# Kernel optimization log

Measured on AMD Instinct MI355X. Metric: run time of the kernel, lower is better.

Reference implementation:

```python
import math
import jax, jax.numpy as jnp
import numpy as np

B, M, N = 32, 64, 5000   # batch, multi_width (POMO rollouts), n_nodes
L, H, D, E = 100, 8, 16, 128  # local_size, head_num, qkv_dim, emb_dim


def setup_inputs() -> dict:
    key = jax.random.key(0)
    ks = jax.random.split(key, 10)
    return {
        "dist": jax.random.uniform(ks[0], (B, M, N), jnp.float32),
        "theta": jax.random.uniform(ks[1], (B, M, N), jnp.float32, minval=-math.pi, maxval=math.pi),
        "ninf_mask": jnp.zeros((B, M, N), jnp.float32),
        "W_init": jax.random.normal(ks[2], (E, 2), jnp.float32) * 0.1,
        "b_init": jax.random.normal(ks[3], (E,), jnp.float32) * 0.1,
        "cur_token": jax.random.uniform(ks[4], (E,), jnp.float32, minval=-1.0, maxval=1.0),
        "Wq": jax.random.normal(ks[5], (H * D, E), jnp.float32) * 0.05,
        "Wk": jax.random.normal(ks[6], (H * D, E), jnp.float32) * 0.05,
        "Wv": jax.random.normal(ks[7], (H * D, E), jnp.float32) * 0.05,
        "Wc": jax.random.normal(ks[8], (E, H * D), jnp.float32) * 0.05,
        "bc": jax.random.normal(ks[9], (E,), jnp.float32) * 0.05,
    }


def _positional_signal():
    # transformer sinusoidal encoding over the L gathered neighbors (E even -> no pad)
    num_ts = E // 2
    log_inc = math.log(10000.0) / max(num_ts - 1, 1)
    inv_ts = jnp.exp(jnp.arange(num_ts, dtype=jnp.float32) * -log_inc)
    pos = jnp.arange(L, dtype=jnp.float32)
    scaled = pos[:, None] * inv_ts[None, :]            # [L, E/2]
    return jnp.concatenate([jnp.sin(scaled), jnp.cos(scaled)], axis=1)  # [L, E]


def reference(dist, theta, ninf_mask, W_init, b_init, cur_token, Wq, Wk, Wv, Wc, bc):
    # mask out infeasible nodes (dist - (-inf) = +inf pushes them out of top-k)
    d = dist - ninf_mask                               # [B, M, N]
    neg_vals, idx = jax.lax.top_k(-d, L)               # smallest-L distances
    sorted_dist = -neg_vals                            # [B, M, L] ascending
    sorted_mask = jnp.take_along_axis(ninf_mask, idx, axis=-1)
    norm = sorted_dist.max(axis=-1, keepdims=True) + 1e-6
    sorted_dist = sorted_dist / norm
    sorted_theta = jnp.take_along_axis(theta, idx, axis=-1)
    sdt = jnp.stack([sorted_dist, sorted_theta], axis=-1)   # [B, M, L, 2]

    init_k = sdt @ W_init.T + b_init + _positional_signal()  # [B, M, L, E]

    # current-token query is a single shared learned vector -> q is [H, D]
    q = (Wq @ cur_token).reshape(H, D)
    kh = (init_k @ Wk.T).reshape(B, M, L, H, D)
    vh = (init_k @ Wv.T).reshape(B, M, L, H, D)

    score = jnp.einsum('hd,bmlhd->bhml', q, kh) / jnp.sqrt(jnp.float32(D))
    score = score + sorted_mask[:, None, :, :]              # rank3 ninf mask
    w = jax.nn.softmax(score, axis=-1)                      # [B, H, M, L]
    att = jnp.einsum('bhml,bmlhd->bmhd', w, vh).reshape(B, M, H * D)
    mh = att @ Wc.T + bc                                    # [B, M, E]

    score2 = jnp.einsum('bme,bmle->bml', mh, init_k) / jnp.sqrt(jnp.float32(E))

    # scatter local scores back into full [B, M, N]
    bi = jnp.arange(B)[:, None, None]
    mi = jnp.arange(M)[None, :, None]
    out = jnp.zeros((B, M, N), jnp.float32).at[bi, mi, idx].set(score2)
    return out
```

## Files before the change

### kernel.cpp

```cpp
#include <hip/hip_runtime.h>
#include <math.h>

#define B_ 32
#define M_ 64
#define N_ 5000
#define L_ 100
#define H_ 8
#define D_ 16
#define E_ 128
#define NBIN 1024
#define NI4 1250
#define RPB 8

#define OFF_POSQ  0
#define OFF_C0    800
#define OFF_C1    808
#define OFF_C2    816
#define OFF_PV0   824
#define OFF_PV1   952
#define OFF_PVB   1080
#define OFF_WC0   1208
#define OFF_WC1   1336
#define OFF_WCB   1464
#define OFF_SB    1592
#define OFF_PCB   1596
#define OFF_PV    1696
#define OFF_PCT   14496

#define WSYNC() do { asm volatile("s_waitcnt lgkmcnt(0)" ::: "memory"); __builtin_amdgcn_sched_barrier(0); } while (0)
#define VSYNC() do { asm volatile("s_waitcnt vmcnt(0)" ::: "memory"); __builtin_amdgcn_sched_barrier(0); } while (0)

__device__ __forceinline__ int vbin(float v) {
  if (!(v >= 0.f)) return 0;
  if (v >= 1.0f) return NBIN - 1;
  return (int)(v * (float)NBIN);
}
__device__ __forceinline__ unsigned int umap(float v) {
  unsigned int b = __float_as_uint(v);
  return (b & 0x80000000u) ? ~b : (b | 0x80000000u);
}
#define HMAP(b)  ((((b) & 15) << 6) + ((b) >> 4))
#define HMAP4(b) ((((b) & 3) << 6) + ((b) >> 2))

__global__ __launch_bounds__(128) void precomp(
    const float* __restrict__ Wq, const float* __restrict__ Wk,
    const float* __restrict__ cur, const float* __restrict__ Wi,
    const float* __restrict__ bi, const float* __restrict__ Wv,
    const float* __restrict__ Wc, const float* __restrict__ bc,
    float* __restrict__ ws)
{
  const int tid = threadIdx.x;
  const int blk = blockIdx.x;
  __shared__ float pr[E_];
  __shared__ float red[8];
  const int lane = tid & 63, wvv = tid >> 6;

  if (blk == 0) {
    float qsv = 0.f;
    for (int e = 0; e < E_; ++e) qsv = fmaf(Wq[tid * E_ + e], cur[e], qsv);
    float wk0=0,wk1=0,wkb=0,pv0=0,pv1=0,pvb=0,wc0=0,wc1=0,wcb=0;
    for (int e = 0; e < E_; ++e) {
      float wi0 = Wi[2*e], wi1 = Wi[2*e+1], bie = bi[e];
      float wk = Wk[tid*E_+e], wvx = Wv[tid*E_+e], wcc = Wc[e*(H_*D_)+tid];
      wk0=fmaf(wk,wi0,wk0);  wk1=fmaf(wk,wi1,wk1);  wkb=fmaf(wk,bie,wkb);
      pv0=fmaf(wvx,wi0,pv0); pv1=fmaf(wvx,wi1,pv1); pvb=fmaf(wvx,bie,pvb);
      wc0=fmaf(wcc,wi0,wc0); wc1=fmaf(wcc,wi1,wc1); wcb=fmaf(wcc,bie,wcb);
    }
    ws[OFF_PV0+tid]=pv0; ws[OFF_PV1+tid]=pv1; ws[OFF_PVB+tid]=pvb;
    ws[OFF_WC0+tid]=wc0; ws[OFF_WC1+tid]=wc1; ws[OFF_WCB+tid]=wcb;
    float c0 = qsv*wk0, c1 = qsv*wk1, c2 = qsv*wkb;
    for (int off = 1; off < 16; off <<= 1) {
      c0 += __shfl_xor(c0, off, 16); c1 += __shfl_xor(c1, off, 16); c2 += __shfl_xor(c2, off, 16);
    }
    if ((tid & 15) == 0) {
      int h = tid >> 4;
      ws[OFF_C0+h] = c0*0.25f; ws[OFF_C1+h] = c1*0.25f; ws[OFF_C2+h] = c2*0.25f;
    }
    float p0 = Wi[2*tid]*bc[tid], p1 = Wi[2*tid+1]*bc[tid], p2 = bi[tid]*bc[tid];
    for (int off = 32; off > 0; off >>= 1) {
      p0 += __shfl_xor(p0, off, 64); p1 += __shfl_xor(p1, off, 64); p2 += __shfl_xor(p2, off, 64);
    }
    if (lane == 0) { red[wvv*3+0]=p0; red[wvv*3+1]=p1; red[wvv*3+2]=p2; }
    __syncthreads();
    if (tid == 0) {
      ws[OFF_SB+0]=red[0]+red[3]; ws[OFF_SB+1]=red[1]+red[4]; ws[OFF_SB+2]=red[2]+red[5];
    }
  } else {
    const int l = blk - 1;
    const float log_inc = 0.14619588050755848f;
    {
      int j = tid & 63;
      float scaled = (float)l * expf(-(float)j * log_inc);
      pr[tid] = (tid < 64) ? sinf(scaled) : cosf(scaled);
    }
    __syncthreads();
    float qsv=0.f, pwk=0.f, accv=0.f, accc=0.f;
    for (int e = 0; e < E_; ++e) qsv = fmaf(Wq[tid*E_+e], cur[e], qsv);
    for (int e = 0; e < E_; ++e) {
      float p = pr[e];
      pwk  = fmaf(Wk[tid*E_+e], p, pwk);
      accv = fmaf(Wv[tid*E_+e], p, accv);
      accc = fmaf(Wc[e*(H_*D_)+tid], p, accc);
    }
    ws[OFF_PV  + l*(H_*D_) + tid] = accv;
    ws[OFF_PCT + tid*L_ + l] = accc;
    float pq = qsv * pwk;
    for (int off = 1; off < 16; off <<= 1) pq += __shfl_xor(pq, off, 16);
    if ((tid & 15) == 0) ws[OFF_POSQ + (tid>>4)*L_ + l] = pq * 0.25f;
    float pb = pr[tid] * bc[tid];
    for (int off = 32; off > 0; off >>= 1) pb += __shfl_xor(pb, off, 64);
    if (lane == 0) red[wvv] = pb;
    __syncthreads();
    if (tid == 0) ws[OFF_PCB + l] = red[0] + red[1];
  }
}

__global__ __launch_bounds__(512) void local_att_kernel(
    const float* __restrict__ dist, const float* __restrict__ theta,
    const float* __restrict__ ninf, const float* __restrict__ ws,
    float* __restrict__ out)
{
  __shared__ alignas(16) unsigned int arena[RPB][1024];
  __shared__ unsigned int cnt8[RPB];

  const int tid  = threadIdx.x;
  const int lane = tid & 63;
  const int wv   = tid >> 6;
  const size_t base = (size_t)(blockIdx.x * RPB + wv) * N_;
  unsigned int* hist = arena[wv];
  unsigned long long* sel = (unsigned long long*)&arena[wv][256];
  float* sdv = (float*)&arena[wv][520];
  unsigned int* idxs = &arena[wv][648];
  float* stv = (float*)&arena[wv][776];
  float* smv = (float*)&arena[wv][876];
  float* att = (float*)&arena[wv][0];

  const float4* d4 = (const float4*)(dist + base);
  const float4* n4 = (const float4*)(ninf + base);

#pragma unroll
  for (int k = 0; k < 16; ++k) hist[lane + 64 * k] = 0u;
  WSYNC();

  {
    float4 dreg[20], nreg[20];
#pragma unroll
    for (int t = 0; t < 20; ++t) {
      int i4 = lane + 64 * t;
      if (i4 < NI4) { dreg[t] = d4[i4]; nreg[t] = n4[i4]; }
    }
#pragma unroll
    for (int t = 0; t < 20; ++t) {
      int i4 = lane + 64 * t;
      if (i4 < NI4) {
#pragma unroll
        for (int c = 0; c < 4; ++c) {
          float v = (&dreg[t].x)[c] - (&nreg[t].x)[c];
          atomicAdd(&hist[HMAP(vbin(v))], 1u);
        }
      }
    }
  }
  WSYNC();

  unsigned int bstar, cumB, binc;
  {
    unsigned int s = 0;
#pragma unroll
    for (int k = 0; k < 16; ++k) s += hist[k * 64 + lane];
    unsigned int v = s;
#pragma unroll
    for (int off = 1; off < 64; off <<= 1) {
      unsigned int x = __shfl_up(v, off, 64);
      if (lane >= off) v += x;
    }
    unsigned int cumBefore = v - s;
    bool cross = (cumBefore < (unsigned)L_) && (v >= (unsigned)L_);
    unsigned long long mk = __ballot(cross);
    int src = __ffsll(mk) - 1;
    unsigned int bstarL = 0, cumL = 0, bincL = 0;
    if (cross) {
      unsigned int c = cumBefore; int kk = 0;
      for (; kk < 16; ++kk) {
        unsigned int h = hist[kk * 64 + lane];
        if (c + h >= (unsigned)L_) { bincL = h; break; }
        c += h;
      }
      bstarL = (unsigned)(lane * 16 + kk); cumL = c;
    }
    bstar = (unsigned)__shfl((int)bstarL, src, 64);
    cumB  = (unsigned)__shfl((int)cumL,  src, 64);
    binc  = (unsigned)__shfl((int)bincL, src, 64);
  }
  const bool fb = (cumB + binc > 128u);

  if (!fb) {
    sel[lane] = ~0ull; sel[lane + 64] = ~0ull;
    if (lane == 0) cnt8[wv] = 0u;
    WSYNC();
    float4 dreg[20], nreg[20];
#pragma unroll
    for (int t = 0; t < 20; ++t) {
      int i4 = lane + 64 * t;
      if (i4 < NI4) { dreg[t] = d4[i4]; nreg[t] = n4[i4]; }
    }
#pragma unroll
    for (int t = 0; t < 20; ++t) {
      int i4 = lane + 64 * t;
      if (i4 < NI4) {
#pragma unroll
        for (int c = 0; c < 4; ++c) {
          float v = (&dreg[t].x)[c] - (&nreg[t].x)[c];
          if (vbin(v) <= (int)bstar) {
            unsigned long long key = ((unsigned long long)umap(v) << 16) | (unsigned)(i4 * 4 + c);
            unsigned int p = atomicAdd(&cnt8[wv], 1u);
            if (p < 128u) sel[p] = key;
          }
        }
      }
    }
  } else {
    unsigned long long prefix = 0ull;
    unsigned int Krem = L_;
    for (int pass = 0; pass < 6; ++pass) {
      const int shift = 40 - 8 * pass;
#pragma unroll
      for (int k = 0; k < 4; ++k) hist[lane + 64 * k] = 0u;
      WSYNC();
      for (int t = 0; t < 20; ++t) {
        int i4 = lane + 64 * t;
        if (i4 < NI4) {
          float4 dv = d4[i4], nv = n4[i4];
#pragma unroll
          for (int c = 0; c < 4; ++c) {
            float v = (&dv.x)[c] - (&nv.x)[c];
            unsigned long long key = ((unsigned long long)umap(v) << 16) | (unsigned)(i4 * 4 + c);
            if ((key >> (shift + 8)) == prefix)
              atomicAdd(&hist[HMAP4((int)((key >> shift) & 0xFFu))], 1u);
          }
        }
      }
      WSYNC();
      unsigned int s4 = 0;
#pragma unroll
      for (int k = 0; k < 4; ++k) s4 += hist[k * 64 + lane];
      unsigned int v2 = s4;
#pragma unroll
      for (int off = 1; off < 64; off <<= 1) {
        unsigned int x = __shfl_up(v2, off, 64);
        if (lane >= off) v2 += x;
      }
      unsigned int cb = v2 - s4;
      bool cr = (cb < Krem) && (v2 >= Krem);
      unsigned long long mk2 = __ballot(cr);
      int sl = __ffsll(mk2) - 1;
      unsigned int chL = 0, cmL = 0;
      if (cr) {
        unsigned int c = cb; int kk = 0;
        for (; kk < 4; ++kk) {
          unsigned int h = hist[kk * 64 + lane];
          if (c + h >= Krem) break;
          c += h;
        }
        chL = (unsigned)(lane * 4 + kk); cmL = c;
      }
      unsigned int chosen = (unsigned)__shfl((int)chL, sl, 64);
      unsigned int cum2   = (unsigned)__shfl((int)cmL, sl, 64);
      prefix = (prefix << 8) | chosen;
      Krem -= cum2;
      WSYNC();
    }
    const unsigned long long kpiv = prefix;
    sel[lane] = ~0ull; sel[lane + 64] = ~0ull;
    if (lane == 0) cnt8[wv] = 0u;
    WSYNC();
    for (int t = 0; t < 20; ++t) {
      int i4 = lane + 64 * t;
      if (i4 < NI4) {
        float4 dv = d4[i4], nv = n4[i4];
#pragma unroll
        for (int c = 0; c < 4; ++c) {
          float v = (&dv.x)[c] - (&nv.x)[c];
          unsigned long long key = ((unsigned long long)umap(v) << 16) | (unsigned)(i4 * 4 + c);
          if (key <= kpiv) {
            unsigned int p = atomicAdd(&cnt8[wv], 1u);
            if (p < 128u) sel[p] = key;
          }
        }
      }
    }
  }
  WSYNC();

  {
    unsigned long long ka = sel[lane], kb = sel[lane + 64];
    int ra = 0, rb = 0;
#pragma unroll 8
    for (int j2 = 0; j2 < 128; ++j2) {
      unsigned long long kj = sel[j2];
      ra += (kj < ka) ? 1 : 0;
      rb += (kj < kb) ? 1 : 0;
    }
    if (ka != ~0ull) {
      unsigned int u = (unsigned int)(ka >> 16);
      unsigned int bits = (u & 0x80000000u) ? (u ^ 0x80000000u) : ~u;
      sdv[ra] = __uint_as_float(bits);
      idxs[ra] = (unsigned int)(ka & 0xFFFFull);
    }
    if (kb != ~0ull) {
      unsigned int u = (unsigned int)(kb >> 16);
      unsigned int bits = (u & 0x80000000u) ? (u ^ 0x80000000u) : ~u;
      sdv[rb] = __uint_as_float(bits);
      idxs[rb] = (unsigned int)(kb & 0xFFFFull);
    }
  }
  WSYNC();

  const float invn = 1.0f / (sdv[L_ - 1] + 1e-6f);
  {
    const int l1 = lane + 64;
    const int l1g = (l1 < L_) ? l1 : 0;
    unsigned int i0 = idxs[lane], i1 = idxs[l1g];
    float sd0 = sdv[lane], sd1 = sdv[l1g];
    float th0 = theta[base + i0];
    float nm0 = ninf[base + i0];
    float th1 = 0.f, nm1 = 0.f;
    if (l1 < L_) { th1 = theta[base + i1]; nm1 = ninf[base + i1]; }
    stv[lane] = th0; smv[lane] = nm0; sdv[lane] = sd0 * invn;
    if (l1 < L_) { stv[l1] = th1; smv[l1] = nm1; sdv[l1] = sd1 * invn; }
  }
  WSYNC();

  const int hh = lane >> 3, jj = lane & 7;
  float w13[13];
  float a0, a1;
  {
    const float c0 = ws[OFF_C0 + hh], c1 = ws[OFF_C1 + hh], c2 = ws[OFF_C2 + hh];
    float mx = -INFINITY;
#pragma unroll
    for (int k = 0; k < 13; ++k) {
      int l = jj + 8 * k;
      float scv = -INFINITY;
      if (l < L_)
        scv = fmaf(sdv[l], c0, fmaf(stv[l], c1, c2 + ws[OFF_POSQ + hh * L_ + l] + smv[l]));
      w13[k] = scv;
      mx = fmaxf(mx, scv);
    }
#pragma unroll
    for (int off = 1; off <= 4; off <<= 1) mx = fmaxf(mx, __shfl_xor(mx, off, 64));
    float sum = 0.f;
#pragma unroll
    for (int k = 0; k < 13; ++k) { float e = expf(w13[k] - mx); w13[k] = e; sum += e; }
#pragma unroll
    for (int off = 1; off <= 4; off <<= 1) sum += __shfl_xor(sum, off, 64);
    const float inv = 1.0f / sum;
    a0 = 0.f; a1 = 0.f;
#pragma unroll
    for (int k = 0; k < 13; ++k) {
      int l = jj + 8 * k; int lc = (l < L_) ? l : 0;
      float wgt = w13[k] * inv; w13[k] = wgt;
      a0 = fmaf(wgt, sdv[lc], a0);
      a1 = fmaf(wgt, stv[lc], a1);
    }
#pragma unroll
    for (int off = 1; off <= 4; off <<= 1) { a0 += __shfl_xor(a0, off, 64); a1 += __shfl_xor(a1, off, 64); }
  }

  {
    float part[16];
#pragma unroll
    for (int t = 0; t < 16; ++t) part[t] = 0.f;
#pragma unroll
    for (int k = 0; k < 13; ++k) {
      int l = jj + 8 * k;
      if (l < L_) {
        const float* pv = ws + OFF_PV + l * (H_ * D_) + hh * 16;
        float wgt = w13[k];
#pragma unroll
        for (int t = 0; t < 16; ++t) part[t] = fmaf(wgt, pv[t], part[t]);
      }
    }
#pragma unroll
    for (int off = 1; off <= 4; off <<= 1) {
#pragma unroll
      for (int t = 0; t < 16; ++t) part[t] += __shfl_xor(part[t], off, 64);
    }
#pragma unroll
    for (int t = 0; t < 16; ++t) {
      int hd = hh * 16 + t;
      att[hd] = fmaf(a0, ws[OFF_PV0 + hd], fmaf(a1, ws[OFF_PV1 + hd], ws[OFF_PVB + hd])) + part[t];
    }
  }
  WSYNC();

  float m0, m1, mb;
  {
    float x0 = att[lane], x1 = att[lane + 64];
    m0 = fmaf(x0, ws[OFF_WC0 + lane], x1 * ws[OFF_WC0 + lane + 64]);
    m1 = fmaf(x0, ws[OFF_WC1 + lane], x1 * ws[OFF_WC1 + lane + 64]);
    mb = fmaf(x0, ws[OFF_WCB + lane], x1 * ws[OFF_WCB + lane + 64]);
#pragma unroll
    for (int off = 1; off < 64; off <<= 1) {
      m0 += __shfl_xor(m0, off, 64);
      m1 += __shfl_xor(m1, off, 64);
      mb += __shfl_xor(mb, off, 64);
    }
    m0 += ws[OFF_SB + 0]; m1 += ws[OFF_SB + 1]; mb += ws[OFF_SB + 2];
  }

  const int l1 = lane + 64;
  const int l1c = (l1 < L_) ? l1 : 0;
  float s2a = 0.f, s2b = 0.f;
#pragma unroll 8
  for (int hd = 0; hd < H_ * D_; ++hd) {
    float a = att[hd];
    s2a = fmaf(a, ws[OFF_PCT + hd * L_ + lane], s2a);
    s2b = fmaf(a, ws[OFF_PCT + hd * L_ + l1c], s2b);
  }
  const float SC = 0.08838834764831845f;
  float out_a = (fmaf(sdv[lane], m0, fmaf(stv[lane], m1, mb)) + ws[OFF_PCB + lane] + s2a) * SC;
  float out_b = (fmaf(sdv[l1c], m0, fmaf(stv[l1c], m1, mb)) + ws[OFF_PCB + l1c] + s2b) * SC;
  unsigned int ia = idxs[lane];
  unsigned int ib = idxs[l1c];

  {
    float4* o4 = (float4*)(out + base);
    const float4 z = make_float4(0.f, 0.f, 0.f, 0.f);
#pragma unroll
    for (int t = 0; t < 20; ++t) {
      int i4 = lane + 64 * t;
      if (i4 < NI4) o4[i4] = z;
    }
  }
  VSYNC();
  out[base + ia] = out_a;
  if (l1 < L_) out[base + ib] = out_b;
}

extern "C" void kernel_launch(void* const* d_in, const int* in_sizes, int n_in,
                              void* d_out, int out_size, void* d_ws, size_t ws_size,
                              hipStream_t stream) {
  const float* dist = (const float*)d_in[0];
  const float* theta = (const float*)d_in[1];
  const float* ninf = (const float*)d_in[2];
  const float* Wi   = (const float*)d_in[3];
  const float* bi   = (const float*)d_in[4];
  const float* cur  = (const float*)d_in[5];
  const float* Wq   = (const float*)d_in[6];
  const float* Wk   = (const float*)d_in[7];
  const float* Wv   = (const float*)d_in[8];
  const float* Wc   = (const float*)d_in[9];
  const float* bcv  = (const float*)d_in[10];
  float* out = (float*)d_out;
  float* ws  = (float*)d_ws;

  precomp<<<dim3(L_ + 1), dim3(128), 0, stream>>>(Wq, Wk, cur, Wi, bi, Wv, Wc, bcv, ws);
  local_att_kernel<<<dim3((B_ * M_) / RPB), dim3(512), 0, stream>>>(dist, theta, ninf, ws, out);
}
```

Measured before the change: 79.76 us.

## Process one row per 128-thread block with register-cached keys and single-pass output

The main kernel now gives each row a 128-thread block instead of one wave per row in a 512-thread block. Each thread keeps the mapped distance keys in registers, so the selection and fallback radix passes no longer reload dist and ninf from global memory. Output is written in one pass: a shared bitmap and hash table merge the scattered scores with the zero fill, replacing a zero store followed by scattered stores. The cost is block-wide barriers and shared atomics in place of wave-local sync, plus more registers per thread.

Measured after the change: 72.08 us. 1.11x faster.

```diff
diff --git a/kernel.cpp b/kernel.cpp
--- a/kernel.cpp
+++ b/kernel.cpp
@@ -10,7 +10,7 @@
 #define E_ 128
 #define NBIN 1024
 #define NI4 1250
-#define RPB 8
+#define NT 128
 
 #define OFF_POSQ  0
 #define OFF_C0    800
@@ -27,9 +27,6 @@
 #define OFF_PV    1696
 #define OFF_PCT   14496
 
-#define WSYNC() do { asm volatile("s_waitcnt lgkmcnt(0)" ::: "memory"); __builtin_amdgcn_sched_barrier(0); } while (0)
-#define VSYNC() do { asm volatile("s_waitcnt vmcnt(0)" ::: "memory"); __builtin_amdgcn_sched_barrier(0); } while (0)
-
 __device__ __forceinline__ int vbin(float v) {
   if (!(v >= 0.f)) return 0;
   if (v >= 1.0f) return NBIN - 1;
@@ -39,8 +36,12 @@
   unsigned int b = __float_as_uint(v);
   return (b & 0x80000000u) ? ~b : (b | 0x80000000u);
 }
-#define HMAP(b)  ((((b) & 15) << 6) + ((b) >> 4))
-#define HMAP4(b) ((((b) & 3) << 6) + ((b) >> 2))
+__device__ __forceinline__ float unmap(unsigned int u) {
+  unsigned int b = (u & 0x80000000u) ? (u ^ 0x80000000u) : ~u;
+  return __uint_as_float(b);
+}
+#define HMAP8(b) ((((b) & 7) << 7) | ((b) >> 3))
+#define HMAP2(b) ((((b) & 1) << 7) | ((b) >> 1))
 
 __global__ __launch_bounds__(128) void precomp(
     const float* __restrict__ Wq, const float* __restrict__ Wk,
@@ -115,106 +116,89 @@
   }
 }
 
-__global__ __launch_bounds__(512) void local_att_kernel(
+__global__ __launch_bounds__(NT, 4) void local_att_kernel(
     const float* __restrict__ dist, const float* __restrict__ theta,
     const float* __restrict__ ninf, const float* __restrict__ ws,
     float* __restrict__ out)
 {
-  __shared__ alignas(16) unsigned int arena[RPB][1024];
-  __shared__ unsigned int cnt8[RPB];
-
-  const int tid  = threadIdx.x;
-  const int lane = tid & 63;
-  const int wv   = tid >> 6;
-  const size_t base = (size_t)(blockIdx.x * RPB + wv) * N_;
-  unsigned int* hist = arena[wv];
-  unsigned long long* sel = (unsigned long long*)&arena[wv][256];
-  float* sdv = (float*)&arena[wv][520];
-  unsigned int* idxs = &arena[wv][648];
-  float* stv = (float*)&arena[wv][776];
-  float* smv = (float*)&arena[wv][876];
-  float* att = (float*)&arena[wv][0];
-
+  __shared__ unsigned int hist[NBIN];
+  __shared__ unsigned long long sel[128];
+  __shared__ float sdv[128];
+  __shared__ unsigned int idxs[128];
+  __shared__ float stv[L_], smv[L_];
+  __shared__ float att[H_ * D_];
+  __shared__ unsigned int bitmap[160];
+  __shared__ unsigned int hidx[256];
+  __shared__ float hval[256];
+  __shared__ unsigned int wsum[2];
+  __shared__ unsigned int s_bstar, s_cumB, s_binc, s_cnt, s_chosen, s_cumb2;
+
+  const int tid = threadIdx.x;
+  const int lane = tid & 63, wv = tid >> 6;
+  const size_t base = (size_t)blockIdx.x * N_;
   const float4* d4 = (const float4*)(dist + base);
   const float4* n4 = (const float4*)(ninf + base);
 
-#pragma unroll
-  for (int k = 0; k < 16; ++k) hist[lane + 64 * k] = 0u;
-  WSYNC();
-
-  {
-    float4 dreg[20], nreg[20];
-#pragma unroll
-    for (int t = 0; t < 20; ++t) {
-      int i4 = lane + 64 * t;
-      if (i4 < NI4) { dreg[t] = d4[i4]; nreg[t] = n4[i4]; }
-    }
-#pragma unroll
-    for (int t = 0; t < 20; ++t) {
-      int i4 = lane + 64 * t;
-      if (i4 < NI4) {
-#pragma unroll
-        for (int c = 0; c < 4; ++c) {
-          float v = (&dreg[t].x)[c] - (&nreg[t].x)[c];
-          atomicAdd(&hist[HMAP(vbin(v))], 1u);
-        }
-      }
-    }
-  }
-  WSYNC();
-
-  unsigned int bstar, cumB, binc;
+  for (int j = tid; j < NBIN; j += NT) hist[j] = 0u;
+  sel[tid] = ~0ull;
+  if (tid == 0) s_cnt = 0u;
+  __syncthreads();
+
+  unsigned int u[40];
+#pragma unroll
+  for (int t = 0; t < 10; ++t) {
+    int i4 = tid + NT * t;
+    if (i4 < NI4) {
+      float4 dv = d4[i4], nv = n4[i4];
+#pragma unroll
+      for (int c = 0; c < 4; ++c) {
+        float v = (&dv.x)[c] - (&nv.x)[c];
+        u[4 * t + c] = umap(v);
+        atomicAdd(&hist[HMAP8(vbin(v))], 1u);
+      }
+    }
+  }
+  __syncthreads();
+
   {
     unsigned int s = 0;
 #pragma unroll
-    for (int k = 0; k < 16; ++k) s += hist[k * 64 + lane];
+    for (int k = 0; k < 8; ++k) s += hist[(k << 7) | tid];
     unsigned int v = s;
 #pragma unroll
     for (int off = 1; off < 64; off <<= 1) {
       unsigned int x = __shfl_up(v, off, 64);
       if (lane >= off) v += x;
     }
+    if (lane == 63) wsum[wv] = v;
+    __syncthreads();
+    if (wv == 1) v += wsum[0];
     unsigned int cumBefore = v - s;
-    bool cross = (cumBefore < (unsigned)L_) && (v >= (unsigned)L_);
-    unsigned long long mk = __ballot(cross);
-    int src = __ffsll(mk) - 1;
-    unsigned int bstarL = 0, cumL = 0, bincL = 0;
-    if (cross) {
-      unsigned int c = cumBefore; int kk = 0;
-      for (; kk < 16; ++kk) {
-        unsigned int h = hist[kk * 64 + lane];
-        if (c + h >= (unsigned)L_) { bincL = h; break; }
+    if (cumBefore < (unsigned)L_ && v >= (unsigned)L_) {
+      unsigned int c = cumBefore;
+#pragma unroll
+      for (int k = 0; k < 8; ++k) {
+        unsigned int h = hist[(k << 7) | tid];
+        if (c + h >= (unsigned)L_) { s_bstar = tid * 8 + k; s_cumB = c; s_binc = h; break; }
         c += h;
       }
-      bstarL = (unsigned)(lane * 16 + kk); cumL = c;
-    }
-    bstar = (unsigned)__shfl((int)bstarL, src, 64);
-    cumB  = (unsigned)__shfl((int)cumL,  src, 64);
-    binc  = (unsigned)__shfl((int)bincL, src, 64);
-  }
-  const bool fb = (cumB + binc > 128u);
+    }
+    __syncthreads();
+  }
+  const int bstar = (int)s_bstar;
+  const bool fb = (s_cumB + s_binc > 128u);
 
   if (!fb) {
-    sel[lane] = ~0ull; sel[lane + 64] = ~0ull;
-    if (lane == 0) cnt8[wv] = 0u;
-    WSYNC();
-    float4 dreg[20], nreg[20];
-#pragma unroll
-    for (int t = 0; t < 20; ++t) {
-      int i4 = lane + 64 * t;
-      if (i4 < NI4) { dreg[t] = d4[i4]; nreg[t] = n4[i4]; }
-    }
-#pragma unroll
-    for (int t = 0; t < 20; ++t) {
-      int i4 = lane + 64 * t;
+#pragma unroll
+    for (int t = 0; t < 10; ++t) {
+      int i4 = tid + NT * t;
       if (i4 < NI4) {
 #pragma unroll
         for (int c = 0; c < 4; ++c) {
-          float v = (&dreg[t].x)[c] - (&nreg[t].x)[c];
-          if (vbin(v) <= (int)bstar) {
-            unsigned long long key = ((unsigned long long)umap(v) << 16) | (unsigned)(i4 * 4 + c);
-            unsigned int p = atomicAdd(&cnt8[wv], 1u);
-            if (p < 128u) sel[p] = key;
+          unsigned int uu = u[4 * t + c];
+          if (vbin(unmap(uu)) <= bstar) {
+            unsigned int p = atomicAdd(&s_cnt, 1u);
+            if (p < 128u) sel[p] = ((unsigned long long)uu << 16) | (unsigned)(4 * i4 + c);
           }
         }
       }
@@ -224,174 +208,149 @@
     unsigned int Krem = L_;
     for (int pass = 0; pass < 6; ++pass) {
       const int shift = 40 - 8 * pass;
-#pragma unroll
-      for (int k = 0; k < 4; ++k) hist[lane + 64 * k] = 0u;
-      WSYNC();
-      for (int t = 0; t < 20; ++t) {
-        int i4 = lane + 64 * t;
+      for (int j = tid; j < 256; j += NT) hist[j] = 0u;
+      __syncthreads();
+#pragma unroll
+      for (int t = 0; t < 10; ++t) {
+        int i4 = tid + NT * t;
         if (i4 < NI4) {
-          float4 dv = d4[i4], nv = n4[i4];
 #pragma unroll
           for (int c = 0; c < 4; ++c) {
-            float v = (&dv.x)[c] - (&nv.x)[c];
-            unsigned long long key = ((unsigned long long)umap(v) << 16) | (unsigned)(i4 * 4 + c);
-            if ((key >> (shift + 8)) == prefix)
-              atomicAdd(&hist[HMAP4((int)((key >> shift) & 0xFFu))], 1u);
+            unsigned long long key = ((unsigned long long)u[4 * t + c] << 16) | (unsigned)(4 * i4 + c);
+            if ((key >> (shift + 8)) == prefix) {
+              unsigned int b = (unsigned int)(key >> shift) & 0xFFu;
+              atomicAdd(&hist[HMAP2(b)], 1u);
+            }
           }
         }
       }
-      WSYNC();
-      unsigned int s4 = 0;
-#pragma unroll
-      for (int k = 0; k < 4; ++k) s4 += hist[k * 64 + lane];
-      unsigned int v2 = s4;
+      __syncthreads();
+      unsigned int s0 = hist[tid];
+      unsigned int s1 = hist[128 + tid];
+      unsigned int s = s0 + s1;
+      unsigned int v = s;
 #pragma unroll
       for (int off = 1; off < 64; off <<= 1) {
-        unsigned int x = __shfl_up(v2, off, 64);
-        if (lane >= off) v2 += x;
-      }
-      unsigned int cb = v2 - s4;
-      bool cr = (cb < Krem) && (v2 >= Krem);
-      unsigned long long mk2 = __ballot(cr);
-      int sl = __ffsll(mk2) - 1;
-      unsigned int chL = 0, cmL = 0;
-      if (cr) {
-        unsigned int c = cb; int kk = 0;
-        for (; kk < 4; ++kk) {
-          unsigned int h = hist[kk * 64 + lane];
-          if (c + h >= Krem) break;
-          c += h;
-        }
-        chL = (unsigned)(lane * 4 + kk); cmL = c;
-      }
-      unsigned int chosen = (unsigned)__shfl((int)chL, sl, 64);
-      unsigned int cum2   = (unsigned)__shfl((int)cmL, sl, 64);
-      prefix = (prefix << 8) | chosen;
-      Krem -= cum2;
-      WSYNC();
+        unsigned int x = __shfl_up(v, off, 64);
+        if (lane >= off) v += x;
+      }
+      if (lane == 63) wsum[wv] = v;
+      __syncthreads();
+      if (wv == 1) v += wsum[0];
+      unsigned int cb = v - s;
+      if (cb < Krem && v >= Krem) {
+        if (cb + s0 >= Krem) { s_chosen = 2u * tid;     s_cumb2 = cb; }
+        else                 { s_chosen = 2u * tid + 1; s_cumb2 = cb + s0; }
+      }
+      __syncthreads();
+      prefix = (prefix << 8) | s_chosen;
+      Krem -= s_cumb2;
+      __syncthreads();
     }
     const unsigned long long kpiv = prefix;
-    sel[lane] = ~0ull; sel[lane + 64] = ~0ull;
-    if (lane == 0) cnt8[wv] = 0u;
-    WSYNC();
-    for (int t = 0; t < 20; ++t) {
-      int i4 = lane + 64 * t;
+#pragma unroll
+    for (int t = 0; t < 10; ++t) {
+      int i4 = tid + NT * t;
       if (i4 < NI4) {
-        float4 dv = d4[i4], nv = n4[i4];
 #pragma unroll
         for (int c = 0; c < 4; ++c) {
-          float v = (&dv.x)[c] - (&nv.x)[c];
-          unsigned long long key = ((unsigned long long)umap(v) << 16) | (unsigned)(i4 * 4 + c);
+          unsigned long long key = ((unsigned long long)u[4 * t + c] << 16) | (unsigned)(4 * i4 + c);
           if (key <= kpiv) {
-            unsigned int p = atomicAdd(&cnt8[wv], 1u);
+            unsigned int p = atomicAdd(&s_cnt, 1u);
             if (p < 128u) sel[p] = key;
           }
         }
       }
     }
   }
-  WSYNC();
+  __syncthreads();
 
   {
-    unsigned long long ka = sel[lane], kb = sel[lane + 64];
-    int ra = 0, rb = 0;
+    unsigned long long ka = sel[tid];
+    int ra = 0;
 #pragma unroll 8
-    for (int j2 = 0; j2 < 128; ++j2) {
-      unsigned long long kj = sel[j2];
-      ra += (kj < ka) ? 1 : 0;
-      rb += (kj < kb) ? 1 : 0;
-    }
+    for (int j = 0; j < 128; ++j) ra += (sel[j] < ka) ? 1 : 0;
     if (ka != ~0ull) {
-      unsigned int u = (unsigned int)(ka >> 16);
-      unsigned int bits = (u & 0x80000000u) ? (u ^ 0x80000000u) : ~u;
-      sdv[ra] = __uint_as_float(bits);
+      unsigned int uu = (unsigned int)(ka >> 16);
+      sdv[ra] = unmap(uu);
       idxs[ra] = (unsigned int)(ka & 0xFFFFull);
     }
-    if (kb != ~0ull) {
-      unsigned int u = (unsigned int)(kb >> 16);
-      unsigned int bits = (u & 0x80000000u) ? (u ^ 0x80000000u) : ~u;
-      sdv[rb] = __uint_as_float(bits);
-      idxs[rb] = (unsigned int)(kb & 0xFFFFull);
-    }
-  }
-  WSYNC();
+  }
+  __syncthreads();
 
   const float invn = 1.0f / (sdv[L_ - 1] + 1e-6f);
-  {
-    const int l1 = lane + 64;
-    const int l1g = (l1 < L_) ? l1 : 0;
-    unsigned int i0 = idxs[lane], i1 = idxs[l1g];
-    float sd0 = sdv[lane], sd1 = sdv[l1g];
-    float th0 = theta[base + i0];
-    float nm0 = ninf[base + i0];
-    float th1 = 0.f, nm1 = 0.f;
-    if (l1 < L_) { th1 = theta[base + i1]; nm1 = ninf[base + i1]; }
-    stv[lane] = th0; smv[lane] = nm0; sdv[lane] = sd0 * invn;
-    if (l1 < L_) { stv[l1] = th1; smv[l1] = nm1; sdv[l1] = sd1 * invn; }
-  }
-  WSYNC();
-
-  const int hh = lane >> 3, jj = lane & 7;
-  float w13[13];
-  float a0, a1;
-  {
-    const float c0 = ws[OFF_C0 + hh], c1 = ws[OFF_C1 + hh], c2 = ws[OFF_C2 + hh];
-    float mx = -INFINITY;
-#pragma unroll
-    for (int k = 0; k < 13; ++k) {
-      int l = jj + 8 * k;
-      float scv = -INFINITY;
-      if (l < L_)
-        scv = fmaf(sdv[l], c0, fmaf(stv[l], c1, c2 + ws[OFF_POSQ + hh * L_ + l] + smv[l]));
-      w13[k] = scv;
-      mx = fmaxf(mx, scv);
-    }
-#pragma unroll
-    for (int off = 1; off <= 4; off <<= 1) mx = fmaxf(mx, __shfl_xor(mx, off, 64));
-    float sum = 0.f;
-#pragma unroll
-    for (int k = 0; k < 13; ++k) { float e = expf(w13[k] - mx); w13[k] = e; sum += e; }
-#pragma unroll
-    for (int off = 1; off <= 4; off <<= 1) sum += __shfl_xor(sum, off, 64);
-    const float inv = 1.0f / sum;
-    a0 = 0.f; a1 = 0.f;
-#pragma unroll
-    for (int k = 0; k < 13; ++k) {
-      int l = jj + 8 * k; int lc = (l < L_) ? l : 0;
-      float wgt = w13[k] * inv; w13[k] = wgt;
-      a0 = fmaf(wgt, sdv[lc], a0);
-      a1 = fmaf(wgt, stv[lc], a1);
-    }
-#pragma unroll
-    for (int off = 1; off <= 4; off <<= 1) { a0 += __shfl_xor(a0, off, 64); a1 += __shfl_xor(a1, off, 64); }
-  }
-
-  {
-    float part[16];
-#pragma unroll
-    for (int t = 0; t < 16; ++t) part[t] = 0.f;
-#pragma unroll
-    for (int k = 0; k < 13; ++k) {
-      int l = jj + 8 * k;
-      if (l < L_) {
-        const float* pv = ws + OFF_PV + l * (H_ * D_) + hh * 16;
-        float wgt = w13[k];
-#pragma unroll
-        for (int t = 0; t < 16; ++t) part[t] = fmaf(wgt, pv[t], part[t]);
-      }
-    }
-#pragma unroll
-    for (int off = 1; off <= 4; off <<= 1) {
-#pragma unroll
-      for (int t = 0; t < 16; ++t) part[t] += __shfl_xor(part[t], off, 64);
-    }
-#pragma unroll
-    for (int t = 0; t < 16; ++t) {
-      int hd = hh * 16 + t;
-      att[hd] = fmaf(a0, ws[OFF_PV0 + hd], fmaf(a1, ws[OFF_PV1 + hd], ws[OFF_PVB + hd])) + part[t];
-    }
-  }
-  WSYNC();
+  if (tid < L_) {
+    unsigned int ix = idxs[tid];
+    stv[tid] = theta[base + ix];
+    smv[tid] = ninf[base + ix];
+  }
+  __syncthreads();
+
+  if (wv == 0) {
+    const int hh = lane >> 3, jj = lane & 7;
+    float w13[13];
+    float a0, a1;
+    {
+      const float c0 = ws[OFF_C0 + hh], c1 = ws[OFF_C1 + hh], c2 = ws[OFF_C2 + hh];
+      float mx = -INFINITY;
+#pragma unroll
+      for (int k = 0; k < 13; ++k) {
+        int l = jj + 8 * k;
+        float scv = -INFINITY;
+        if (l < L_)
+          scv = fmaf(sdv[l] * invn, c0, fmaf(stv[l], c1, c2 + ws[OFF_POSQ + hh * L_ + l] + smv[l]));
+        w13[k] = scv;
+        mx = fmaxf(mx, scv);
+      }
+#pragma unroll
+      for (int off = 1; off <= 4; off <<= 1) mx = fmaxf(mx, __shfl_xor(mx, off, 64));
+      float sum = 0.f;
+#pragma unroll
+      for (int k = 0; k < 13; ++k) { float e = expf(w13[k] - mx); w13[k] = e; sum += e; }
+#pragma unroll
+      for (int off = 1; off <= 4; off <<= 1) sum += __shfl_xor(sum, off, 64);
+      const float inv = 1.0f / sum;
+      a0 = 0.f; a1 = 0.f;
+#pragma unroll
+      for (int k = 0; k < 13; ++k) {
+        int l = jj + 8 * k; int lc = (l < L_) ? l : 0;
+        float wgt = w13[k] * inv; w13[k] = wgt;
+        a0 = fmaf(wgt, sdv[lc] * invn, a0);
+        a1 = fmaf(wgt, stv[lc], a1);
+      }
+#pragma unroll
+      for (int off = 1; off <= 4; off <<= 1) { a0 += __shfl_xor(a0, off, 64); a1 += __shfl_xor(a1, off, 64); }
+    }
+    {
+      float part[16];
+#pragma unroll
+      for (int t = 0; t < 16; ++t) part[t] = 0.f;
+#pragma unroll
+      for (int k = 0; k < 13; ++k) {
+        int l = jj + 8 * k;
+        if (l < L_) {
+          const float* pv = ws + OFF_PV + l * (H_ * D_) + hh * 16;
+          float wgt = w13[k];
+#pragma unroll
+          for (int t = 0; t < 16; ++t) part[t] = fmaf(wgt, pv[t], part[t]);
+        }
+      }
+#pragma unroll
+      for (int off = 1; off <= 4; off <<= 1) {
+#pragma unroll
+        for (int t = 0; t < 16; ++t) part[t] += __shfl_xor(part[t], off, 64);
+      }
+#pragma unroll
+      for (int t = 0; t < 16; ++t) {
+        int hd = hh * 16 + t;
+        att[hd] = fmaf(a0, ws[OFF_PV0 + hd], fmaf(a1, ws[OFF_PV1 + hd], ws[OFF_PVB + hd])) + part[t];
+      }
+    }
+  } else {
+    for (int j = lane; j < 160; j += 64) bitmap[j] = 0u;
+    for (int j = lane; j < 256; j += 64) hidx[j] = 0xFFFFFFFFu;
+  }
+  __syncthreads();
 
   float m0, m1, mb;
   {
@@ -408,33 +367,41 @@
     m0 += ws[OFF_SB + 0]; m1 += ws[OFF_SB + 1]; mb += ws[OFF_SB + 2];
   }
 
-  const int l1 = lane + 64;
-  const int l1c = (l1 < L_) ? l1 : 0;
-  float s2a = 0.f, s2b = 0.f;
+  if (tid < L_) {
+    float acc = ws[OFF_PCB + tid];
 #pragma unroll 8
-  for (int hd = 0; hd < H_ * D_; ++hd) {
-    float a = att[hd];
-    s2a = fmaf(a, ws[OFF_PCT + hd * L_ + lane], s2a);
-    s2b = fmaf(a, ws[OFF_PCT + hd * L_ + l1c], s2b);
-  }
-  const float SC = 0.08838834764831845f;
-  float out_a = (fmaf(sdv[lane], m0, fmaf(stv[lane], m1, mb)) + ws[OFF_PCB + lane] + s2a) * SC;
-  float out_b = (fmaf(sdv[l1c], m0, fmaf(stv[l1c], m1, mb)) + ws[OFF_PCB + l1c] + s2b) * SC;
-  unsigned int ia = idxs[lane];
-  unsigned int ib = idxs[l1c];
-
-  {
-    float4* o4 = (float4*)(out + base);
-    const float4 z = make_float4(0.f, 0.f, 0.f, 0.f);
-#pragma unroll
-    for (int t = 0; t < 20; ++t) {
-      int i4 = lane + 64 * t;
-      if (i4 < NI4) o4[i4] = z;
-    }
-  }
-  VSYNC();
-  out[base + ia] = out_a;
-  if (l1 < L_) out[base + ib] = out_b;
+    for (int hd = 0; hd < H_ * D_; ++hd) acc = fmaf(att[hd], ws[OFF_PCT + hd * L_ + tid], acc);
+    const float SC = 0.08838834764831845f;
+    float s2v = (fmaf(sdv[tid] * invn, m0, fmaf(stv[tid], m1, mb)) + acc) * SC;
+    unsigned int idx = idxs[tid];
+    unsigned int p = idx & 255u;
+    while (atomicCAS(&hidx[p], 0xFFFFFFFFu, idx) != 0xFFFFFFFFu) p = (p + 1) & 255u;
+    hval[p] = s2v;
+    atomicOr(&bitmap[idx >> 5], 1u << (idx & 31));
+  }
+  __syncthreads();
+
+  float4* o4 = (float4*)(out + base);
+#pragma unroll
+  for (int t = 0; t < 10; ++t) {
+    int i4 = tid + NT * t;
+    if (i4 < NI4) {
+      unsigned int wbits = (bitmap[i4 >> 3] >> ((i4 & 7) * 4)) & 0xFu;
+      float4 o = make_float4(0.f, 0.f, 0.f, 0.f);
+      if (wbits) {
+#pragma unroll
+        for (int c = 0; c < 4; ++c) {
+          if ((wbits >> c) & 1u) {
+            unsigned int idx = (unsigned int)(4 * i4 + c);
+            unsigned int p = idx & 255u;
+            while (hidx[p] != idx) p = (p + 1) & 255u;
+            (&o.x)[c] = hval[p];
+          }
+        }
+      }
+      o4[i4] = o;
+    }
+  }
 }
 
 extern "C" void kernel_launch(void* const* d_in, const int* in_sizes, int n_in,
@@ -455,5 +422,5 @@
   float* ws  = (float*)d_ws;
 
   precomp<<<dim3(L_ + 1), dim3(128), 0, stream>>>(Wq, Wk, cur, Wi, bi, Wv, Wc, bcv, ws);
-  local_att_kernel<<<dim3((B_ * M_) / RPB), dim3(512), 0, stream>>>(dist, theta, ninf, ws, out);
-}
+  local_att_kernel<<<dim3(B_ * M_), dim3(NT), 0, stream>>>(dist, theta, ninf, ws, out);
+}
```
